# Optimization experiments

Hardware: AMD Instinct MI355X
Metric: run time of the kernel (lower is better)

## Reference

```python
import jax, jax.numpy as jnp
import numpy as np

B, N, C, H = 4, 2048, 1024, 16
HD = C // H  # head dim = 64


def setup_inputs() -> dict:
    key = jax.random.key(0)
    k1, k2, k3, k4 = jax.random.split(key, 4)
    x = jax.random.normal(k1, (B, N, C), dtype=jnp.float32)
    # nn.Linear(C, 3C, bias=False): weight [3C, C], y = x @ W.T
    w_qkv = jax.random.normal(k2, (3 * C, C), dtype=jnp.float32) * (C ** -0.5)
    # nn.Linear(C, C) with bias
    w_out = jax.random.normal(k3, (C, C), dtype=jnp.float32) * (C ** -0.5)
    b_out = jax.random.normal(k4, (C,), dtype=jnp.float32) * 0.01
    return {"x": x, "w_qkv": w_qkv, "w_out": w_out, "b_out": b_out}


def reference(x, w_qkv, w_out, b_out):
    scale = HD ** -0.5
    qkv = jnp.einsum('bnc,dc->bnd', x, w_qkv)  # [B, N, 3C]
    q, k, v = jnp.split(qkv, 3, axis=-1)
    # rearrange 'b n (h c) -> b h n c'
    def heads(t):
        return t.reshape(B, N, H, HD).transpose(0, 2, 1, 3)
    q, k, v = heads(q) * scale, heads(k), heads(v)
    scores = jnp.einsum('bhnc,bhmc->bhnm', q, k)  # [B, H, N, N]
    attn = jax.nn.softmax(scores, axis=-1)
    v_hat = jnp.einsum('bhnm,bhmc->bhnc', attn, v)
    out = v_hat.transpose(0, 2, 1, 3).reshape(B, N, C)  # 'b h n c -> b n (h c)'
    return jnp.einsum('bnc,dc->bnd', out, w_out) + b_out
```

## Files before the change

### kernel.cpp

```cpp
#include <hip/hip_runtime.h>

typedef unsigned short ushort_t;
typedef __attribute__((ext_vector_type(8))) short short8;
typedef __attribute__((ext_vector_type(4))) float f32x4;
typedef __attribute__((ext_vector_type(16))) float f32x16;
typedef __attribute__((ext_vector_type(4))) float float4v;
typedef __attribute__((ext_vector_type(4))) unsigned short ushortx4;
typedef __attribute__((ext_vector_type(4))) unsigned int uint4v;

#define AS1 __attribute__((address_space(1)))
#define AS3 __attribute__((address_space(3)))

#define B_ 4
#define N_ 2048
#define C_ 1024
#define H_ 16
#define HD_ 64
#define M_TOT 8192
#define N3_ 3072

#define QSCALE 0.18033688011112042f

__device__ __forceinline__ unsigned short f2bf(float f) {
    unsigned int u = __float_as_uint(f);
    u += 0x7fffu + ((u >> 16) & 1u);
    return (unsigned short)(u >> 16);
}

__global__ __launch_bounds__(256) void cast_f32_bf16(const float* __restrict__ in,
                                                     ushort_t* __restrict__ out, int n4) {
    int i = blockIdx.x * blockDim.x + threadIdx.x;
    int stride = gridDim.x * blockDim.x;
    for (; i < n4; i += stride) {
        float4v v = ((const float4v*)in)[i];
        ushortx4 o;
        o[0] = f2bf(v[0]); o[1] = f2bf(v[1]); o[2] = f2bf(v[2]); o[3] = f2bf(v[3]);
        ((ushortx4*)out)[i] = o;
    }
}


template <int EPI>
__global__ __launch_bounds__(256) void gemm_bt(const ushort_t* __restrict__ A,
                                               const ushort_t* __restrict__ Bw,
                                               ushort_t* __restrict__ o0,
                                               ushort_t* __restrict__ o1,
                                               ushort_t* __restrict__ o2,
                                               float* __restrict__ outf,
                                               const float* __restrict__ bias, int K) {
    __shared__ ushort_t As[2][128 * 32];
    __shared__ ushort_t Bs[2][128 * 32];
    const int tid = threadIdx.x;
    const int lane = tid & 63;
    const int wid = tid >> 6;
    const int l15 = lane & 15, lg = lane >> 4;
    const int wr = wid >> 1, wc = wid & 1;
    const int m0 = blockIdx.y * 128, n0 = blockIdx.x * 128;

    f32x4 acc[4][4] = {};

    auto stage = [&](int buf, int k0) {
        int row = tid >> 2;
        int ko = (tid & 3) * 8;
        const ushort_t* a0 = A + (size_t)(m0 + row) * K + k0 + ko;
        const ushort_t* b0 = Bw + (size_t)(n0 + row) * K + k0 + ko;
        char* la = (char*)(&As[buf][0]) + (tid & 192) * 16;
        char* lb = (char*)(&Bs[buf][0]) + (tid & 192) * 16;
        __builtin_amdgcn_global_load_lds((const AS1 void*)a0, (AS3 void*)la, 16, 0, 0);
        __builtin_amdgcn_global_load_lds((const AS1 void*)(a0 + (size_t)64 * K),
                                         (AS3 void*)(la + 4096), 16, 0, 0);
        __builtin_amdgcn_global_load_lds((const AS1 void*)b0, (AS3 void*)lb, 16, 0, 0);
        __builtin_amdgcn_global_load_lds((const AS1 void*)(b0 + (size_t)64 * K),
                                         (AS3 void*)(lb + 4096), 16, 0, 0);
    };

    stage(0, 0);
    __syncthreads();
    const int NKI = K >> 5;
    for (int kt = 0; kt < NKI; ++kt) {
        const int cur = kt & 1;
        if (kt + 1 < NKI) stage(cur ^ 1, (kt + 1) << 5);
        short8 af[4], bf[4];
#pragma unroll
        for (int mi = 0; mi < 4; ++mi)
            af[mi] = *(const short8*)(&As[cur][(wr * 64 + mi * 16 + l15) * 32 + lg * 8]);
#pragma unroll
        for (int ni = 0; ni < 4; ++ni)
            bf[ni] = *(const short8*)(&Bs[cur][(wc * 64 + ni * 16 + l15) * 32 + lg * 8]);
#pragma unroll
        for (int mi = 0; mi < 4; ++mi)
#pragma unroll
            for (int ni = 0; ni < 4; ++ni)
                acc[mi][ni] = __builtin_amdgcn_mfma_f32_16x16x32_bf16(af[mi], bf[ni],
                                                                      acc[mi][ni], 0, 0, 0);
        __syncthreads();
    }

    if (EPI == 0) {
        const int sel = blockIdx.x >> 3;
        const int cb = (blockIdx.x & 7) * 128 + wc * 64;
#pragma unroll
        for (int mi = 0; mi < 4; ++mi) {
            const int r0 = m0 + wr * 64 + mi * 16 + lg * 4;
            const int b = r0 >> 11, n = r0 & 2047;
            const int blk = n >> 5, nlo = n & 31;
#pragma unroll
            for (int ni = 0; ni < 4; ++ni) {
                const int c = cb + ni * 16 + l15;
                const int h = c >> 6, hd = c & 63;
                const int bh = b * H_ + h;
                f32x4 a = acc[mi][ni];
                if (sel == 2) {
                    size_t base = (((size_t)(bh * 64 + blk) * 2 + (hd >> 5)) * 2 +
                                   ((n >> 4) & 1)) * 512 +
                                  ((hd & 31) + ((n >> 3) & 1) * 32) * 8 + (n & 7);
                    ushortx4 pk;
#pragma unroll
                    for (int j = 0; j < 4; ++j) pk[j] = f2bf(a[j]);
                    *(ushortx4*)(&o2[base]) = pk;
                } else {
                    size_t base = ((size_t)(bh * 64 + blk) * 4 + (hd >> 4)) * 512 +
                                  (nlo + ((hd >> 3) & 1) * 32) * 8 + (hd & 7);
                    if (sel == 0) {
#pragma unroll
                        for (int j = 0; j < 4; ++j) o0[base + j * 8] = f2bf(a[j] * QSCALE);
                    } else {
#pragma unroll
                        for (int j = 0; j < 4; ++j) o1[base + j * 8] = f2bf(a[j]);
                    }
                }
            }
        }
    } else {
#pragma unroll
        for (int ni = 0; ni < 4; ++ni) {
            const int c = n0 + wc * 64 + ni * 16 + l15;
            const float bv = bias[c];
#pragma unroll
            for (int mi = 0; mi < 4; ++mi) {
                const int r0 = m0 + wr * 64 + mi * 16 + lg * 4;
                f32x4 a = acc[mi][ni];
#pragma unroll
                for (int j = 0; j < 4; ++j)
                    outf[(size_t)(r0 + j) * C_ + c] = a[j] + bv;
            }
        }
    }
}

__global__ __launch_bounds__(256, 2) void attn_fwd(const ushort_t* __restrict__ Qf,
                                                   const ushort_t* __restrict__ Kf,
                                                   const ushort_t* __restrict__ Vf,
                                                   ushort_t* __restrict__ Ov) {
    const int tid = threadIdx.x;
    const int lane = tid & 63;
    const int wid = tid >> 6;
    const int lc = lane & 31, lh = lane >> 5;

    const int wg = blockIdx.x;
    const int xcd = wg & 7, slot = wg >> 3;
    const int bh = xcd * 8 + (slot >> 4);
    const int qt = slot & 15;

    const ushort_t* qpb = Qf + (size_t)bh * N_ * HD_;
    const ushort_t* kpb = Kf + (size_t)bh * N_ * HD_ + lane * 8;
    const ushort_t* vpb = Vf + (size_t)bh * N_ * HD_ + lane * 8;

    const int qblk = qt * 4 + wid;

    short8 qf[4];
#pragma unroll
    for (int ks = 0; ks < 4; ++ks)
        qf[ks] = *(const short8*)(qpb + ((size_t)qblk * 4 + ks) * 512 + lane * 8);

    f32x16 oacc[2] = {};
    f32x16 ssum = {};

    uint4v ow;
    ow[0] = 0x3F803F80u; ow[1] = 0x3F803F80u; ow[2] = 0x3F803F80u; ow[3] = 0x3F803F80u;
    const short8 onesf = __builtin_bit_cast(short8, ow);

    short8 kf[4], vf[4];
#pragma unroll
    for (int ks = 0; ks < 4; ++ks) kf[ks] = *(const short8*)(kpb + (size_t)ks * 512);
#pragma unroll
    for (int f = 0; f < 4; ++f) vf[f] = *(const short8*)(vpb + (size_t)f * 512);

    f32x16 saccA = {}, saccB = {};
#pragma unroll
    for (int ks = 0; ks < 4; ++ks)
        saccA = __builtin_amdgcn_mfma_f32_32x32x16_bf16(kf[ks], qf[ks], saccA, 0, 0, 0);
#pragma unroll
    for (int ks = 0; ks < 4; ++ks)
        kf[ks] = *(const short8*)(kpb + (size_t)(4 + ks) * 512);

    const ushort_t* kptr = kpb + (size_t)8 * 512;
    const ushort_t* vptr = vpb + (size_t)4 * 512;

    auto step = [&](f32x16& su, f32x16& sw) {
        f32x16 z = {};
        __builtin_amdgcn_s_setprio(1);
        sw = __builtin_amdgcn_mfma_f32_32x32x16_bf16(kf[0], qf[0], z, 0, 0, 0);
        sw = __builtin_amdgcn_mfma_f32_32x32x16_bf16(kf[1], qf[1], sw, 0, 0, 0);
        sw = __builtin_amdgcn_mfma_f32_32x32x16_bf16(kf[2], qf[2], sw, 0, 0, 0);
        sw = __builtin_amdgcn_mfma_f32_32x32x16_bf16(kf[3], qf[3], sw, 0, 0, 0);
        __builtin_amdgcn_s_setprio(0);
#pragma unroll
        for (int ks = 0; ks < 4; ++ks)
            kf[ks] = *(const short8*)(kptr + (size_t)ks * 512);
        kptr += 4 * 512;

        float p[16];
#pragma unroll
        for (int r = 0; r < 16; ++r) p[r] = __builtin_amdgcn_exp2f(su[r]);

        unsigned pk[4][2];
#pragma unroll
        for (int r1 = 0; r1 < 4; ++r1)
#pragma unroll
            for (int c = 0; c < 2; ++c)
                asm("v_cvt_pk_bf16_f32 %0, %1, %2"
                    : "=v"(pk[r1][c])
                    : "v"(p[4 * r1 + 2 * c]), "v"(p[4 * r1 + 2 * c + 1]));

        short8 pb[2];
#pragma unroll
        for (int kb = 0; kb < 2; ++kb) {
            unsigned a0 = pk[2 * kb][0], b0 = pk[2 * kb + 1][0];
            unsigned a1 = pk[2 * kb][1], b1 = pk[2 * kb + 1][1];
            asm("v_permlane32_swap_b32 %0, %1" : "+v"(a0), "+v"(b0));
            asm("v_permlane32_swap_b32 %0, %1" : "+v"(a1), "+v"(b1));
            uint4v w;
            w[0] = a0; w[1] = a1; w[2] = b0; w[3] = b1;
            pb[kb] = __builtin_bit_cast(short8, w);
        }

        __builtin_amdgcn_s_setprio(1);
        ssum = __builtin_amdgcn_mfma_f32_32x32x16_bf16(onesf, pb[0], ssum, 0, 0, 0);
        ssum = __builtin_amdgcn_mfma_f32_32x32x16_bf16(onesf, pb[1], ssum, 0, 0, 0);
#pragma unroll
        for (int dt = 0; dt < 2; ++dt)
#pragma unroll
            for (int kb = 0; kb < 2; ++kb)
                oacc[dt] = __builtin_amdgcn_mfma_f32_32x32x16_bf16(vf[dt * 2 + kb], pb[kb],
                                                                   oacc[dt], 0, 0, 0);
        __builtin_amdgcn_s_setprio(0);
#pragma unroll
        for (int f = 0; f < 4; ++f) vf[f] = *(const short8*)(vptr + (size_t)f * 512);
        vptr += 4 * 512;
    };

    for (int t2 = 0; t2 < 32; ++t2) {
        step(saccA, saccB);
        step(saccB, saccA);
    }

    const float inv = 1.f / ssum[0];
    const int b = bh >> 4, h = bh & 15;
    const int qg = qblk * 32 + lc;
    ushort_t* orow = Ov + (size_t)(b * N_ + qg) * C_ + h * HD_;
#pragma unroll
    for (int dt = 0; dt < 2; ++dt)
#pragma unroll
        for (int r1 = 0; r1 < 4; ++r1) {
            ushortx4 pkv;
#pragma unroll
            for (int r0 = 0; r0 < 4; ++r0) pkv[r0] = f2bf(oacc[dt][4 * r1 + r0] * inv);
            *(ushortx4*)(orow + dt * 32 + r1 * 8 + lh * 4) = pkv;
        }
}

extern "C" void kernel_launch(void* const* d_in, const int* in_sizes, int n_in,
                              void* d_out, int out_size, void* d_ws, size_t ws_size,
                              hipStream_t stream) {
    const float* x = (const float*)d_in[0];
    const float* wqkv = (const float*)d_in[1];
    const float* wout = (const float*)d_in[2];
    const float* bout = (const float*)d_in[3];
    float* out = (float*)d_out;

    ushort_t* ws = (ushort_t*)d_ws;
    const size_t XN = (size_t)M_TOT * C_;
    const size_t WQN = (size_t)N3_ * C_;
    const size_t WON = (size_t)C_ * C_;
    ushort_t* xbf = ws;
    ushort_t* wqkvb = xbf + XN;
    ushort_t* woutb = wqkvb + WQN;
    ushort_t* karr = woutb + WON;
    ushort_t* varr = karr + XN;
    ushort_t* qarr = varr + XN;
    ushort_t* vhat = xbf;

    cast_f32_bf16<<<2048, 256, 0, stream>>>(x, xbf, (int)(XN / 4));
    cast_f32_bf16<<<1024, 256, 0, stream>>>(wqkv, wqkvb, (int)(WQN / 4));
    cast_f32_bf16<<<512, 256, 0, stream>>>(wout, woutb, (int)(WON / 4));

    gemm_bt<0><<<dim3(24, 64), 256, 0, stream>>>(xbf, wqkvb, qarr, karr, varr,
                                                 nullptr, nullptr, C_);
    attn_fwd<<<1024, 256, 0, stream>>>(qarr, karr, varr, vhat);
    gemm_bt<1><<<dim3(8, 64), 256, 0, stream>>>(vhat, woutb, nullptr, nullptr, nullptr,
                                                out, bout, C_);
}
```

Baseline: 211.5 us.

## Stage shared K/V tiles through double-buffered LDS with global_load_lds

The attention kernel used to have each of the four waves load the full K and V tiles from global memory into registers itself. Now the block stages each 32-key K/V tile once into a double-buffered LDS array using global_load_lds, with each wave loading a quarter. Every wave then reads its fragments from LDS. This is meant to cut redundant global/L2 traffic by 4x, but it adds a block-wide barrier per tile and drops the software pipelining that overlapped the next QK^T MFMA with the softmax of the current tile.

```diff
diff --git a/kernel.cpp b/kernel.cpp
--- a/kernel.cpp
+++ b/kernel.cpp
@@ -152,6 +152,7 @@
                                                    const ushort_t* __restrict__ Kf,
                                                    const ushort_t* __restrict__ Vf,
                                                    ushort_t* __restrict__ Ov) {
+    __shared__ ushort_t kvlds[2][8 * 512];
     const int tid = threadIdx.x;
     const int lane = tid & 63;
     const int wid = tid >> 6;
@@ -163,8 +164,8 @@
     const int qt = slot & 15;
 
     const ushort_t* qpb = Qf + (size_t)bh * N_ * HD_;
-    const ushort_t* kpb = Kf + (size_t)bh * N_ * HD_ + lane * 8;
-    const ushort_t* vpb = Vf + (size_t)bh * N_ * HD_ + lane * 8;
+    const ushort_t* kpb = Kf + (size_t)bh * N_ * HD_;
+    const ushort_t* vpb = Vf + (size_t)bh * N_ * HD_;
 
     const int qblk = qt * 4 + wid;
 
@@ -180,39 +181,41 @@
     ow[0] = 0x3F803F80u; ow[1] = 0x3F803F80u; ow[2] = 0x3F803F80u; ow[3] = 0x3F803F80u;
     const short8 onesf = __builtin_bit_cast(short8, ow);
 
-    short8 kf[4], vf[4];
-#pragma unroll
-    for (int ks = 0; ks < 4; ++ks) kf[ks] = *(const short8*)(kpb + (size_t)ks * 512);
-#pragma unroll
-    for (int f = 0; f < 4; ++f) vf[f] = *(const short8*)(vpb + (size_t)f * 512);
-
-    f32x16 saccA = {}, saccB = {};
-#pragma unroll
-    for (int ks = 0; ks < 4; ++ks)
-        saccA = __builtin_amdgcn_mfma_f32_32x32x16_bf16(kf[ks], qf[ks], saccA, 0, 0, 0);
-#pragma unroll
-    for (int ks = 0; ks < 4; ++ks)
-        kf[ks] = *(const short8*)(kpb + (size_t)(4 + ks) * 512);
-
-    const ushort_t* kptr = kpb + (size_t)8 * 512;
-    const ushort_t* vptr = vpb + (size_t)4 * 512;
-
-    auto step = [&](f32x16& su, f32x16& sw) {
-        f32x16 z = {};
+    auto stage = [&](int buf, int t) {
+        const ushort_t* bsrc = (wid < 2) ? kpb : vpb;
+        const int coff = (wid & 1) * 2;
+        const ushort_t* s0 = bsrc + ((size_t)t * 4 + coff) * 512 + lane * 8;
+        ushort_t* d0 = &kvlds[buf][(wid * 2) * 512];
+        __builtin_amdgcn_global_load_lds((const AS1 void*)s0, (AS3 void*)d0, 16, 0, 0);
+        __builtin_amdgcn_global_load_lds((const AS1 void*)(s0 + 512), (AS3 void*)(d0 + 512),
+                                         16, 0, 0);
+    };
+
+    stage(0, 0);
+    __syncthreads();
+
+    for (int t = 0; t < 64; ++t) {
+        const int cur = t & 1;
+        if (t < 63) stage(cur ^ 1, t + 1);
+
+        short8 kf[4], vf[4];
+#pragma unroll
+        for (int ks = 0; ks < 4; ++ks)
+            kf[ks] = *(const short8*)(&kvlds[cur][ks * 512 + lane * 8]);
+#pragma unroll
+        for (int f = 0; f < 4; ++f)
+            vf[f] = *(const short8*)(&kvlds[cur][(4 + f) * 512 + lane * 8]);
+
+        f32x16 sacc = {};
         __builtin_amdgcn_s_setprio(1);
-        sw = __builtin_amdgcn_mfma_f32_32x32x16_bf16(kf[0], qf[0], z, 0, 0, 0);
-        sw = __builtin_amdgcn_mfma_f32_32x32x16_bf16(kf[1], qf[1], sw, 0, 0, 0);
-        sw = __builtin_amdgcn_mfma_f32_32x32x16_bf16(kf[2], qf[2], sw, 0, 0, 0);
-        sw = __builtin_amdgcn_mfma_f32_32x32x16_bf16(kf[3], qf[3], sw, 0, 0, 0);
+#pragma unroll
+        for (int ks = 0; ks < 4; ++ks)
+            sacc = __builtin_amdgcn_mfma_f32_32x32x16_bf16(kf[ks], qf[ks], sacc, 0, 0, 0);
         __builtin_amdgcn_s_setprio(0);
-#pragma unroll
-        for (int ks = 0; ks < 4; ++ks)
-            kf[ks] = *(const short8*)(kptr + (size_t)ks * 512);
-        kptr += 4 * 512;
 
         float p[16];
 #pragma unroll
-        for (int r = 0; r < 16; ++r) p[r] = __builtin_amdgcn_exp2f(su[r]);
+        for (int r = 0; r < 16; ++r) p[r] = __builtin_amdgcn_exp2f(sacc[r]);
 
         unsigned pk[4][2];
 #pragma unroll
@@ -245,14 +248,7 @@
                 oacc[dt] = __builtin_amdgcn_mfma_f32_32x32x16_bf16(vf[dt * 2 + kb], pb[kb],
                                                                    oacc[dt], 0, 0, 0);
         __builtin_amdgcn_s_setprio(0);
-#pragma unroll
-        for (int f = 0; f < 4; ++f) vf[f] = *(const short8*)(vptr + (size_t)f * 512);
-        vptr += 4 * 512;
-    };
-
-    for (int t2 = 0; t2 < 32; ++t2) {
-        step(saccA, saccB);
-        step(saccB, saccA);
+        __syncthreads();
     }
 
     const float inv = 1.f / ssum[0];
```

Measured after the change: 202.7 us. 4.2% less time.
